# Kernel optimization log

Measured on AMD Instinct MI355X. Metric: run time of the kernel, lower is better.

The kernel has to match this reference:

```python
import jax, jax.numpy as jnp
import numpy as np

N = 16000      # nodes
E = 256000     # edges (avg degree 16)
C = 64         # channel multiplicity (64x0e node feats)
A = 10         # num elements (one-hot node_attrs)
R = 8          # num radial edge feats
OFFS = [0, 1, 4, 9]   # m-offsets for l=0,1,2 blocks (dims 1,3,5)
AVG_NEIGH = 16.0


def setup_inputs() -> dict:
    key = jax.random.key(0)
    ks = jax.random.split(key, 12)
    species = jax.random.randint(ks[0], (N,), 0, A)
    node_attrs = jax.nn.one_hot(species, A, dtype=jnp.float32)
    node_feats = jax.random.normal(ks[1], (N, C), jnp.float32)
    edge_attrs_real = jax.random.normal(ks[2], (E, 9), jnp.float32)
    edge_attrs_imag = jax.random.normal(ks[3], (E, 9), jnp.float32)
    edge_feats = jax.random.normal(ks[4], (E, R), jnp.float32)
    senders = jax.random.randint(ks[5], (E,), 0, N)
    receivers = jax.random.randint(ks[6], (E,), 0, N)
    # learned parameters
    W_up = jax.random.normal(ks[7], (C, C), jnp.float32)            # linear_up (64x0e -> 64x0e)
    W_tpw = jax.random.normal(ks[8], (A, R, 3, C), jnp.float32) * 0.1  # TensorProductWeightsBlock, weight_numel = 3*C
    W_lin = jax.random.normal(ks[9], (3, C, C), jnp.float32)        # per-l linear on irreps_mid -> irreps_out
    W_skip = jax.random.normal(ks[10], (C, A, C), jnp.float32)      # FullyConnectedTensorProduct skip
    return {"node_attrs": node_attrs, "node_feats": node_feats,
            "edge_attrs_real": edge_attrs_real, "edge_attrs_imag": edge_attrs_imag,
            "edge_feats": edge_feats, "senders": senders, "receivers": receivers,
            "W_up": W_up, "W_tpw": W_tpw, "W_lin": W_lin, "W_skip": W_skip}


def reference(node_attrs, node_feats, edge_attrs_real, edge_attrs_imag, edge_feats,
              senders, receivers, W_up, W_tpw, W_lin, W_skip):
    # skip connection: FullyConnectedTensorProduct(node_feats, node_attrs) (all scalars)
    sc = jnp.einsum('nu,na,uak->nk', node_feats, node_attrs, W_skip) / np.float32(np.sqrt(C * A))
    # linear_up (e3nn Linear with 1/sqrt(fan_in) normalization)
    h = (node_feats @ W_up) / np.float32(np.sqrt(C))
    # per-edge TP weights: einsum('be,ba,aek->bk'), reshaped to [E, 3 paths, C]
    tp_w = jnp.einsum('er,ea,arlu->elu', edge_feats, node_attrs[senders], W_tpw)
    x_s = h[senders]  # gather sender node feats [E, C]
    def conv(edge_attrs):
        # uvu tensor product 64x0e x (0e+1o+2e): CG(0,l,l)=1 -> weighted outer product per l
        parts = [x_s[:, :, None] * tp_w[:, l, :, None] * edge_attrs[:, None, OFFS[l]:OFFS[l + 1]]
                 for l in range(3)]
        mji = jnp.concatenate(parts, axis=-1)                      # [E, C, 9]
        m = jax.ops.segment_sum(mji, receivers, num_segments=N)   # scatter-sum -> [N, C, 9]
        outs = [jnp.einsum('num,uv->nvm', m[:, :, OFFS[l]:OFFS[l + 1]], W_lin[l]) / np.float32(np.sqrt(C))
                for l in range(3)]
        return jnp.concatenate(outs, axis=-1) / np.float32(AVG_NEIGH)  # [N, C, 9]
    message_real = conv(edge_attrs_real)
    message_imag = conv(edge_attrs_imag)
    # torch.view_as_complex + reshape_irreps -> complex [N, C, 9]; returned as (real, imag)
    return message_real, message_imag, sc
```

## Files before the change

kernel.cpp:

```cpp
#include <hip/hip_runtime.h>
#include <hip/hip_bf16.h>

#define NN 16000
#define EE 256000
#define CC 64
#define AA 10
#define RR 8
#define NC9 9216000
#define SC_OFF 18432000

#define WS_H        0
#define WS_BLK      4096000
#define WS_WLT      32768256
#define WS_SPECIES  32817408
#define WS_COUNTS   32881408
#define WS_CURSOR   32945408
#define WS_OFFSETS  33009408
#define WS_PERM     33073472
#define WS_DSTART   33137472
#define WS_DEGCUR   33137728

__device__ __forceinline__ float comp4(float4 v, int j) {
  return j == 0 ? v.x : j == 1 ? v.y : j == 2 ? v.z : v.w;
}

__global__ __launch_bounds__(256) void prep_kernel(
    const float* __restrict__ attrs, const int* __restrict__ recv,
    const float* __restrict__ W_lin, const float* __restrict__ nf,
    const float* __restrict__ W_up, const float* __restrict__ W_skip,
    int* __restrict__ species, int* __restrict__ counts,
    float* __restrict__ wlt, float* __restrict__ h, float* __restrict__ out) {
  __shared__ float sW[4096];
  for (int t = threadIdx.x; t < 4096; t += 256) sW[t] = W_up[t];
  __syncthreads();
  int i = blockIdx.x * 256 + threadIdx.x;
  if (i < NN) {
    const float* p = attrs + (size_t)i * AA;
    int sp = 0;
#pragma unroll
    for (int a = 1; a < AA; ++a)
      if (p[a] > 0.5f) sp = a;
    species[i] = sp;
  }
  if (i < 3 * 64 * 64) {
    int l = i >> 12, rem = i & 4095, v = rem >> 6, u = rem & 63;
    wlt[i] = W_lin[l * 4096 + u * 64 + v];
  }
  if (i < EE) atomicAdd(&counts[recv[i]], 1);
  int wid = __builtin_amdgcn_readfirstlane(threadIdx.x >> 6);
  int lane = threadIdx.x & 63;
  for (int n = blockIdx.x * 4 + wid; n < NN; n += 4000) {
    const float* ap = attrs + (size_t)n * AA;
    int a = 0;
#pragma unroll
    for (int j = 1; j < AA; ++j)
      if (ap[j] > 0.5f) a = j;
    const float* nfp = nf + (size_t)n * 64;
    const float* wsk = W_skip + (size_t)a * 64;
    float hacc = 0.f, sacc = 0.f;
#pragma unroll
    for (int u = 0; u < 64; ++u) {
      float x = nfp[u];
      hacc = fmaf(x, sW[u * 64 + lane], hacc);
      sacc = fmaf(x, wsk[u * 640 + lane], sacc);
    }
    h[(size_t)n * 64 + lane] = hacc * 0.125f;
    out[SC_OFF + (size_t)n * 64 + lane] = sacc * 0.03952847075210474f;
  }
}

__global__ __launch_bounds__(1024) void scan_kernel(
    const int* __restrict__ counts, int* __restrict__ offsets,
    int* __restrict__ dstart, int* __restrict__ degcur) {
  __shared__ int part[1024];
  __shared__ int hist[64];
  int tid = threadIdx.x;
  if (tid < 64) { hist[tid] = 0; degcur[tid] = 0; }
  const int CH = 16;
  int base = tid * CH;
  int loc[CH];
  int s = 0;
#pragma unroll
  for (int i = 0; i < CH; ++i) {
    int idx = base + i;
    int c = (idx < NN) ? counts[idx] : 0;
    loc[i] = c;
    s += c;
  }
  part[tid] = s;
  __syncthreads();
  for (int off = 1; off < 1024; off <<= 1) {
    int t = part[tid];
    int add = (tid >= off) ? part[tid - off] : 0;
    __syncthreads();
    part[tid] = t + add;
    __syncthreads();
  }
  int pre = (tid > 0) ? part[tid - 1] : 0;
#pragma unroll
  for (int i = 0; i < CH; ++i) {
    int idx = base + i;
    if (idx <= NN) offsets[idx] = pre;
    pre += loc[i];
    if (idx < NN) atomicAdd(&hist[min(loc[i], 63)], 1);
  }
  __syncthreads();
  if (tid == 0) {
    int run = 0;
    for (int d = 63; d >= 0; --d) { dstart[d] = run; run += hist[d]; }
  }
}

__global__ __launch_bounds__(256) void edge_kernel(
    const int* __restrict__ recv, const int* __restrict__ senders,
    const int* __restrict__ species, const int* __restrict__ offsets,
    int* __restrict__ cursor, const int* __restrict__ counts,
    const int* __restrict__ dstart, int* __restrict__ degcur,
    int* __restrict__ perm, const float* __restrict__ ef,
    const float* __restrict__ ear, const float* __restrict__ eai,
    float* __restrict__ blk) {
  int e = blockIdx.x * 256 + threadIdx.x;
  if (e < NN) {
    int d = min(counts[e], 63);
    int pos = atomicAdd(&degcur[d], 1);
    perm[dstart[d] + pos] = e;
  }
  if (e >= EE) return;
  int r = recv[e];
  int pos = atomicAdd(&cursor[r], 1);
  int slot = offsets[r] + pos;
  int s = senders[e];
  int a = species[s];
  const float* efp = ef + (size_t)e * 8;
  const float* erp = ear + (size_t)e * 9;
  const float* eip = eai + (size_t)e * 9;
  float4* dst = (float4*)(blk + (size_t)slot * 28);
  float4 q;
  q.x = __int_as_float(s | (a << 20)); q.y = efp[0]; q.z = efp[1]; q.w = efp[2];
  dst[0] = q;
  q.x = efp[3]; q.y = efp[4]; q.z = efp[5]; q.w = efp[6];
  dst[1] = q;
  q.x = efp[7]; q.y = erp[0]; q.z = erp[1]; q.w = erp[2];
  dst[2] = q;
  q.x = erp[3]; q.y = erp[4]; q.z = erp[5]; q.w = erp[6];
  dst[3] = q;
  q.x = erp[7]; q.y = erp[8]; q.z = eip[0]; q.w = eip[1];
  dst[4] = q;
  q.x = eip[2]; q.y = eip[3]; q.z = eip[4]; q.w = eip[5];
  dst[5] = q;
  q.x = eip[6]; q.y = eip[7]; q.z = eip[8]; q.w = 0.f;
  dst[6] = q;
}

#define RLF(V, L) __int_as_float(__builtin_amdgcn_readlane((V), (L)))

#define EDGE2(EFA, ERA, EIA, PKV, XS) do {                                 \
  int a_ = (PKV) >> 20;                                                    \
  const float4* wp_ = (const float4*)(lds + a_ * 1792 + lane * 28);        \
  float4 w_[6];                                                            \
  _Pragma("unroll") for (int g_ = 0; g_ < 6; ++g_) w_[g_] = wp_[gpi[g_]];  \
  float t0_ = 0.f, t1_ = 0.f, t2_ = 0.f;                                   \
  _Pragma("unroll") for (int r_ = 0; r_ < 8; ++r_) {                       \
    t0_ = fmaf((EFA)[r_], comp4(w_[(r_ * 3 + 0) >> 2], (r_ * 3 + 0) & 3), t0_); \
    t1_ = fmaf((EFA)[r_], comp4(w_[(r_ * 3 + 1) >> 2], (r_ * 3 + 1) & 3), t1_); \
    t2_ = fmaf((EFA)[r_], comp4(w_[(r_ * 3 + 2) >> 2], (r_ * 3 + 2) & 3), t2_); \
  }                                                                        \
  t0_ *= (XS); t1_ *= (XS); t2_ *= (XS);                                   \
  accR[0] = fmaf(t0_, (ERA)[0], accR[0]);                                  \
  accI[0] = fmaf(t0_, (EIA)[0], accI[0]);                                  \
  _Pragma("unroll") for (int m_ = 1; m_ < 4; ++m_) {                       \
    accR[m_] = fmaf(t1_, (ERA)[m_], accR[m_]);                             \
    accI[m_] = fmaf(t1_, (EIA)[m_], accI[m_]);                             \
  }                                                                        \
  _Pragma("unroll") for (int m_ = 4; m_ < 9; ++m_) {                       \
    accR[m_] = fmaf(t2_, (ERA)[m_], accR[m_]);                             \
    accI[m_] = fmaf(t2_, (EIA)[m_], accI[m_]);                             \
  }                                                                        \
} while (0)

#define MIXL(LV, M0, M1)                                                    \
  _Pragma("unroll") for (int q_ = 0; q_ < 16; ++q_) {                       \
    float4 w4_ = *(const float4*)&lds[(LV) * 4096 + lane * 64 +             \
                                      ((q_ + lane) & 15) * 4];              \
    _Pragma("unroll") for (int j_ = 0; j_ < 4; ++j_) {                      \
      float wu_ = comp4(w4_, j_);                                           \
      _Pragma("unroll") for (int m_ = (M0); m_ < (M1); ++m_) {              \
        outR[m_] = fmaf(RLF(__float_as_int(accR[m_]), q_ * 4 + j_), wu_, outR[m_]); \
        outI[m_] = fmaf(RLF(__float_as_int(accI[m_]), q_ * 4 + j_), wu_, outI[m_]); \
      }                                                                     \
    }                                                                       \
  }

__global__ __launch_bounds__(512, 4) void fused_kernel(
    const float* __restrict__ h, const int* __restrict__ offs,
    const float* __restrict__ blkd, const int* __restrict__ perm,
    const float* __restrict__ W_tpw, const float* __restrict__ wlt,
    float* __restrict__ out) {
  __shared__ float lds[17920];
  for (int t = threadIdx.x; t < AA * 6 * 64; t += 512) {
    int a = t / 384, rem = t - a * 384;
    int g = rem >> 6, u = rem & 63;
    int gp = (g + 5 * u) % 7;
    const float* src = W_tpw + a * 1536 + g * 256 + u;
    float4 w;
    w.x = src[0]; w.y = src[64]; w.z = src[128]; w.w = src[192];
    *(float4*)&lds[a * 1792 + u * 28 + gp * 4] = w;
  }
  __syncthreads();
  int wid = __builtin_amdgcn_readfirstlane(threadIdx.x >> 6);
  int lane = threadIdx.x & 63;
  int n = __builtin_amdgcn_readfirstlane(perm[blockIdx.x * 8 + wid]);
  int gpi[6];
#pragma unroll
  for (int g = 0; g < 6; ++g) gpi[g] = (g + 5 * lane) % 7;
  float accR[9], accI[9];
#pragma unroll
  for (int m = 0; m < 9; ++m) { accR[m] = 0.f; accI[m] = 0.f; }
  int beg = __builtin_amdgcn_readfirstlane(offs[n]);
  int end_ = __builtin_amdgcn_readfirstlane(offs[n + 1]);
  if (end_ > beg) {
    const int* bi = (const int*)blkd;
    int pk0 = bi[(size_t)beg * 28];
    int pk1 = (beg + 1 < end_) ? bi[(size_t)(beg + 1) * 28] : pk0;
    float xs0 = h[(size_t)(pk0 & 0xFFFFF) * 64 + lane];
    float xs1 = h[(size_t)(pk1 & 0xFFFFF) * 64 + lane];
    float efc[8], erc[9], eic[9];
    {
      const float* ep = blkd + (size_t)beg * 28;
#pragma unroll
      for (int i = 0; i < 8; ++i) efc[i] = ep[1 + i];
#pragma unroll
      for (int i = 0; i < 9; ++i) erc[i] = ep[9 + i];
#pragma unroll
      for (int i = 0; i < 9; ++i) eic[i] = ep[18 + i];
    }
    for (int idx = beg; idx < end_; ++idx) {
      int pk2 = pk0;
      float xs2 = 0.f;
      if (idx + 2 < end_) {
        pk2 = bi[(size_t)(idx + 2) * 28];
        xs2 = h[(size_t)(pk2 & 0xFFFFF) * 64 + lane];
      }
      float efn[8], ern[9], ein[9];
      if (idx + 1 < end_) {
        const float* ep = blkd + (size_t)(idx + 1) * 28;
#pragma unroll
        for (int i = 0; i < 8; ++i) efn[i] = ep[1 + i];
#pragma unroll
        for (int i = 0; i < 9; ++i) ern[i] = ep[9 + i];
#pragma unroll
        for (int i = 0; i < 9; ++i) ein[i] = ep[18 + i];
      } else {
#pragma unroll
        for (int i = 0; i < 8; ++i) efn[i] = 0.f;
#pragma unroll
        for (int i = 0; i < 9; ++i) { ern[i] = 0.f; ein[i] = 0.f; }
      }
      EDGE2(efc, erc, eic, pk0, xs0);
      pk0 = pk1; xs0 = xs1;
      pk1 = pk2; xs1 = xs2;
#pragma unroll
      for (int i = 0; i < 8; ++i) efc[i] = efn[i];
#pragma unroll
      for (int i = 0; i < 9; ++i) { erc[i] = ern[i]; eic[i] = ein[i]; }
    }
  }
  __builtin_amdgcn_sched_barrier(0);
  __syncthreads();
  for (int t = threadIdx.x; t < 3072; t += 512) {
    int l = t >> 10, rem = t & 1023, v = rem >> 4, q = rem & 15;
    int slot = (q + v) & 15;
    float4 w = *(const float4*)(wlt + l * 4096 + v * 64 + q * 4);
    *(float4*)&lds[l * 4096 + v * 64 + slot * 4] = w;
  }
  __syncthreads();
  float outR[9], outI[9];
#pragma unroll
  for (int m = 0; m < 9; ++m) { outR[m] = 0.f; outI[m] = 0.f; }
  MIXL(0, 0, 1)
  MIXL(1, 1, 4)
  MIXL(2, 4, 9)
  const float SCL = 0.0078125f;
  float* stg = lds + 12288 + wid * 576;
#pragma unroll
  for (int m = 0; m < 9; ++m) stg[lane * 9 + m] = outR[m] * SCL;
  __builtin_amdgcn_s_waitcnt(0);
#pragma unroll
  for (int k = 0; k < 9; ++k)
    out[(size_t)n * 576 + k * 64 + lane] = stg[k * 64 + lane];
#pragma unroll
  for (int m = 0; m < 9; ++m) stg[lane * 9 + m] = outI[m] * SCL;
  __builtin_amdgcn_s_waitcnt(0);
#pragma unroll
  for (int k = 0; k < 9; ++k)
    out[NC9 + (size_t)n * 576 + k * 64 + lane] = stg[k * 64 + lane];
}

extern "C" void kernel_launch(void* const* d_in, const int* in_sizes, int n_in,
                              void* d_out, int out_size, void* d_ws, size_t ws_size,
                              hipStream_t stream) {
  const float* node_attrs = (const float*)d_in[0];
  const float* node_feats = (const float*)d_in[1];
  const float* ear        = (const float*)d_in[2];
  const float* eai        = (const float*)d_in[3];
  const float* ef         = (const float*)d_in[4];
  const int*   senders    = (const int*)d_in[5];
  const int*   receivers  = (const int*)d_in[6];
  const float* W_up       = (const float*)d_in[7];
  const float* W_tpw      = (const float*)d_in[8];
  const float* W_lin      = (const float*)d_in[9];
  const float* W_skip     = (const float*)d_in[10];
  float* out = (float*)d_out;

  char* ws = (char*)d_ws;
  float* h        = (float*)(ws + WS_H);
  float* blk      = (float*)(ws + WS_BLK);
  float* wlt      = (float*)(ws + WS_WLT);
  int*   species  = (int*)(ws + WS_SPECIES);
  int*   counts   = (int*)(ws + WS_COUNTS);
  int*   cursor   = (int*)(ws + WS_CURSOR);
  int*   offsets  = (int*)(ws + WS_OFFSETS);
  int*   perm     = (int*)(ws + WS_PERM);
  int*   dstart   = (int*)(ws + WS_DSTART);
  int*   degcur   = (int*)(ws + WS_DEGCUR);

  hipMemsetAsync(ws + WS_COUNTS, 0, 128000, stream);

  prep_kernel<<<1000, 256, 0, stream>>>(node_attrs, receivers, W_lin,
                                        node_feats, W_up, W_skip,
                                        species, counts, wlt, h, out);
  scan_kernel<<<1, 1024, 0, stream>>>(counts, offsets, dstart, degcur);
  edge_kernel<<<1000, 256, 0, stream>>>(receivers, senders, species, offsets,
                                        cursor, counts, dstart, degcur, perm,
                                        ef, ear, eai, blk);
  fused_kernel<<<2000, 512, 0, stream>>>(h, offsets, blk, perm, W_tpw, wlt,
                                         out);
}
```

Measured before the change: 351.6 us.

## Replace packed per-edge block with edge index and gather edge data in fused kernel

The edge kernel no longer copies edge features and edge attributes into a 28-float sorted block. It writes only an (edge id, sender|species) pair per slot, and the fused kernel reads ef/ear/eai directly by edge id, broadcasting them with readfirstlane. This cuts the write and re-read of about 28 MB of staging data, but turns the fused kernel's edge reads into scattered, non-sequential loads and drops the software prefetch of edge data. The change also splits the node linear/skip work into its own one-wave-per-node kernel, drops the LDS swizzle on the TP weights, and adds a sync in the scan kernel.

```diff
diff --git a/kernel.cpp b/kernel.cpp
--- a/kernel.cpp
+++ b/kernel.cpp
@@ -10,29 +10,27 @@
 #define SC_OFF 18432000
 
 #define WS_H        0
-#define WS_BLK      4096000
-#define WS_WLT      32768256
-#define WS_SPECIES  32817408
-#define WS_COUNTS   32881408
-#define WS_CURSOR   32945408
-#define WS_OFFSETS  33009408
-#define WS_PERM     33073472
-#define WS_DSTART   33137472
-#define WS_DEGCUR   33137728
+#define WS_EP2      4096000
+#define WS_WLT      6144000
+#define WS_SPECIES  6193152
+#define WS_COUNTS   6257152
+#define WS_CURSOR   6321152
+#define WS_OFFSETS  6385152
+#define WS_PERM     6449216
+#define WS_DSTART   6513216
+#define WS_DEGCUR   6513472
 
 __device__ __forceinline__ float comp4(float4 v, int j) {
   return j == 0 ? v.x : j == 1 ? v.y : j == 2 ? v.z : v.w;
 }
+__device__ __forceinline__ float rflf(float v) {
+  return __int_as_float(__builtin_amdgcn_readfirstlane(__float_as_int(v)));
+}
 
 __global__ __launch_bounds__(256) void prep_kernel(
     const float* __restrict__ attrs, const int* __restrict__ recv,
-    const float* __restrict__ W_lin, const float* __restrict__ nf,
-    const float* __restrict__ W_up, const float* __restrict__ W_skip,
-    int* __restrict__ species, int* __restrict__ counts,
-    float* __restrict__ wlt, float* __restrict__ h, float* __restrict__ out) {
-  __shared__ float sW[4096];
-  for (int t = threadIdx.x; t < 4096; t += 256) sW[t] = W_up[t];
-  __syncthreads();
+    const float* __restrict__ W_lin, int* __restrict__ species,
+    int* __restrict__ counts, float* __restrict__ wlt) {
   int i = blockIdx.x * 256 + threadIdx.x;
   if (i < NN) {
     const float* p = attrs + (size_t)i * AA;
@@ -47,26 +45,35 @@
     wlt[i] = W_lin[l * 4096 + u * 64 + v];
   }
   if (i < EE) atomicAdd(&counts[recv[i]], 1);
+}
+
+__global__ __launch_bounds__(256) void node_kernel(
+    const float* __restrict__ nf, const float* __restrict__ attrs,
+    const float* __restrict__ W_up, const float* __restrict__ W_skip,
+    float* __restrict__ h, float* __restrict__ out) {
+  __shared__ float sW[4096];
+  for (int t = threadIdx.x; t < 4096; t += 256) sW[t] = W_up[t];
+  __syncthreads();
   int wid = __builtin_amdgcn_readfirstlane(threadIdx.x >> 6);
   int lane = threadIdx.x & 63;
-  for (int n = blockIdx.x * 4 + wid; n < NN; n += 4000) {
-    const float* ap = attrs + (size_t)n * AA;
-    int a = 0;
-#pragma unroll
-    for (int j = 1; j < AA; ++j)
-      if (ap[j] > 0.5f) a = j;
-    const float* nfp = nf + (size_t)n * 64;
-    const float* wsk = W_skip + (size_t)a * 64;
-    float hacc = 0.f, sacc = 0.f;
-#pragma unroll
-    for (int u = 0; u < 64; ++u) {
-      float x = nfp[u];
-      hacc = fmaf(x, sW[u * 64 + lane], hacc);
-      sacc = fmaf(x, wsk[u * 640 + lane], sacc);
-    }
-    h[(size_t)n * 64 + lane] = hacc * 0.125f;
-    out[SC_OFF + (size_t)n * 64 + lane] = sacc * 0.03952847075210474f;
-  }
+  int n = blockIdx.x * 4 + wid;
+  if (n >= NN) return;
+  const float* ap = attrs + (size_t)n * AA;
+  int a = 0;
+#pragma unroll
+  for (int j = 1; j < AA; ++j)
+    if (ap[j] > 0.5f) a = j;
+  const float* nfp = nf + (size_t)n * 64;
+  const float* wsk = W_skip + (size_t)a * 64;
+  float hacc = 0.f, sacc = 0.f;
+#pragma unroll
+  for (int u = 0; u < 64; ++u) {
+    float x = nfp[u];
+    hacc = fmaf(x, sW[u * 64 + lane], hacc);
+    sacc = fmaf(x, wsk[u * 640 + lane], sacc);
+  }
+  h[(size_t)n * 64 + lane] = hacc * 0.125f;
+  out[SC_OFF + (size_t)n * 64 + lane] = sacc * 0.03952847075210474f;
 }
 
 __global__ __launch_bounds__(1024) void scan_kernel(
@@ -76,6 +83,7 @@
   __shared__ int hist[64];
   int tid = threadIdx.x;
   if (tid < 64) { hist[tid] = 0; degcur[tid] = 0; }
+  __syncthreads();
   const int CH = 16;
   int base = tid * CH;
   int loc[CH];
@@ -116,9 +124,7 @@
     const int* __restrict__ species, const int* __restrict__ offsets,
     int* __restrict__ cursor, const int* __restrict__ counts,
     const int* __restrict__ dstart, int* __restrict__ degcur,
-    int* __restrict__ perm, const float* __restrict__ ef,
-    const float* __restrict__ ear, const float* __restrict__ eai,
-    float* __restrict__ blk) {
+    int* __restrict__ perm, int2* __restrict__ ep2) {
   int e = blockIdx.x * 256 + threadIdx.x;
   if (e < NN) {
     int d = min(counts[e], 63);
@@ -131,52 +137,42 @@
   int slot = offsets[r] + pos;
   int s = senders[e];
   int a = species[s];
-  const float* efp = ef + (size_t)e * 8;
-  const float* erp = ear + (size_t)e * 9;
-  const float* eip = eai + (size_t)e * 9;
-  float4* dst = (float4*)(blk + (size_t)slot * 28);
-  float4 q;
-  q.x = __int_as_float(s | (a << 20)); q.y = efp[0]; q.z = efp[1]; q.w = efp[2];
-  dst[0] = q;
-  q.x = efp[3]; q.y = efp[4]; q.z = efp[5]; q.w = efp[6];
-  dst[1] = q;
-  q.x = efp[7]; q.y = erp[0]; q.z = erp[1]; q.w = erp[2];
-  dst[2] = q;
-  q.x = erp[3]; q.y = erp[4]; q.z = erp[5]; q.w = erp[6];
-  dst[3] = q;
-  q.x = erp[7]; q.y = erp[8]; q.z = eip[0]; q.w = eip[1];
-  dst[4] = q;
-  q.x = eip[2]; q.y = eip[3]; q.z = eip[4]; q.w = eip[5];
-  dst[5] = q;
-  q.x = eip[6]; q.y = eip[7]; q.z = eip[8]; q.w = 0.f;
-  dst[6] = q;
-}
-
-#define RLF(V, L) __int_as_float(__builtin_amdgcn_readlane((V), (L)))
-
-#define EDGE2(EFA, ERA, EIA, PKV, XS) do {                                 \
-  int a_ = (PKV) >> 20;                                                    \
+  ep2[slot] = make_int2(e, s | (a << 20));
+}
+
+#define EDGE3(RC, XS) do {                                                 \
+  int e_ = (RC).x;                                                         \
+  int a_ = (RC).y >> 20;                                                   \
+  const float* efp_ = ef + (size_t)e_ * 8;          \
+  const float* erp_ = ear + (size_t)e_ * 9;                                \
+  const float* eip_ = eai + (size_t)e_ * 9;                                \
+  float efs_[8], ers_[9], eis_[9];                                         \
+  _Pragma("unroll") for (int i_ = 0; i_ < 8; ++i_) efs_[i_] = rflf(efp_[i_]); \
+  _Pragma("unroll") for (int i_ = 0; i_ < 9; ++i_) ers_[i_] = rflf(erp_[i_]); \
+  _Pragma("unroll") for (int i_ = 0; i_ < 9; ++i_) eis_[i_] = rflf(eip_[i_]); \
   const float4* wp_ = (const float4*)(lds + a_ * 1792 + lane * 28);        \
   float4 w_[6];                                                            \
-  _Pragma("unroll") for (int g_ = 0; g_ < 6; ++g_) w_[g_] = wp_[gpi[g_]];  \
+  _Pragma("unroll") for (int g_ = 0; g_ < 6; ++g_) w_[g_] = wp_[g_];       \
   float t0_ = 0.f, t1_ = 0.f, t2_ = 0.f;                                   \
   _Pragma("unroll") for (int r_ = 0; r_ < 8; ++r_) {                       \
-    t0_ = fmaf((EFA)[r_], comp4(w_[(r_ * 3 + 0) >> 2], (r_ * 3 + 0) & 3), t0_); \
-    t1_ = fmaf((EFA)[r_], comp4(w_[(r_ * 3 + 1) >> 2], (r_ * 3 + 1) & 3), t1_); \
-    t2_ = fmaf((EFA)[r_], comp4(w_[(r_ * 3 + 2) >> 2], (r_ * 3 + 2) & 3), t2_); \
+    t0_ = fmaf(efs_[r_], comp4(w_[(r_ * 3 + 0) >> 2], (r_ * 3 + 0) & 3), t0_); \
+    t1_ = fmaf(efs_[r_], comp4(w_[(r_ * 3 + 1) >> 2], (r_ * 3 + 1) & 3), t1_); \
+    t2_ = fmaf(efs_[r_], comp4(w_[(r_ * 3 + 2) >> 2], (r_ * 3 + 2) & 3), t2_); \
   }                                                                        \
   t0_ *= (XS); t1_ *= (XS); t2_ *= (XS);                                   \
-  accR[0] = fmaf(t0_, (ERA)[0], accR[0]);                                  \
-  accI[0] = fmaf(t0_, (EIA)[0], accI[0]);                                  \
+  accR[0] = fmaf(t0_, ers_[0], accR[0]);                                   \
+  accI[0] = fmaf(t0_, eis_[0], accI[0]);                                   \
   _Pragma("unroll") for (int m_ = 1; m_ < 4; ++m_) {                       \
-    accR[m_] = fmaf(t1_, (ERA)[m_], accR[m_]);                             \
-    accI[m_] = fmaf(t1_, (EIA)[m_], accI[m_]);                             \
+    accR[m_] = fmaf(t1_, ers_[m_], accR[m_]);                              \
+    accI[m_] = fmaf(t1_, eis_[m_], accI[m_]);                              \
   }                                                                        \
   _Pragma("unroll") for (int m_ = 4; m_ < 9; ++m_) {                       \
-    accR[m_] = fmaf(t2_, (ERA)[m_], accR[m_]);                             \
-    accI[m_] = fmaf(t2_, (EIA)[m_], accI[m_]);                             \
+    accR[m_] = fmaf(t2_, ers_[m_], accR[m_]);                              \
+    accI[m_] = fmaf(t2_, eis_[m_], accI[m_]);                              \
   }                                                                        \
 } while (0)
+
+#define RLF(V, L) __int_as_float(__builtin_amdgcn_readlane((V), (L)))
 
 #define MIXL(LV, M0, M1)                                                    \
   _Pragma("unroll") for (int q_ = 0; q_ < 16; ++q_) {                       \
@@ -193,76 +189,43 @@
 
 __global__ __launch_bounds__(512, 4) void fused_kernel(
     const float* __restrict__ h, const int* __restrict__ offs,
-    const float* __restrict__ blkd, const int* __restrict__ perm,
-    const float* __restrict__ W_tpw, const float* __restrict__ wlt,
-    float* __restrict__ out) {
+    const int2* __restrict__ ep2, const int* __restrict__ perm,
+    const float* __restrict__ ef, const float* __restrict__ ear,
+    const float* __restrict__ eai, const float* __restrict__ W_tpw,
+    const float* __restrict__ wlt, float* __restrict__ out) {
   __shared__ float lds[17920];
   for (int t = threadIdx.x; t < AA * 6 * 64; t += 512) {
     int a = t / 384, rem = t - a * 384;
     int g = rem >> 6, u = rem & 63;
-    int gp = (g + 5 * u) % 7;
     const float* src = W_tpw + a * 1536 + g * 256 + u;
     float4 w;
     w.x = src[0]; w.y = src[64]; w.z = src[128]; w.w = src[192];
-    *(float4*)&lds[a * 1792 + u * 28 + gp * 4] = w;
+    *(float4*)&lds[a * 1792 + u * 28 + g * 4] = w;
   }
   __syncthreads();
   int wid = __builtin_amdgcn_readfirstlane(threadIdx.x >> 6);
   int lane = threadIdx.x & 63;
   int n = __builtin_amdgcn_readfirstlane(perm[blockIdx.x * 8 + wid]);
-  int gpi[6];
-#pragma unroll
-  for (int g = 0; g < 6; ++g) gpi[g] = (g + 5 * lane) % 7;
   float accR[9], accI[9];
 #pragma unroll
   for (int m = 0; m < 9; ++m) { accR[m] = 0.f; accI[m] = 0.f; }
   int beg = __builtin_amdgcn_readfirstlane(offs[n]);
   int end_ = __builtin_amdgcn_readfirstlane(offs[n + 1]);
   if (end_ > beg) {
-    const int* bi = (const int*)blkd;
-    int pk0 = bi[(size_t)beg * 28];
-    int pk1 = (beg + 1 < end_) ? bi[(size_t)(beg + 1) * 28] : pk0;
-    float xs0 = h[(size_t)(pk0 & 0xFFFFF) * 64 + lane];
-    float xs1 = h[(size_t)(pk1 & 0xFFFFF) * 64 + lane];
-    float efc[8], erc[9], eic[9];
-    {
-      const float* ep = blkd + (size_t)beg * 28;
-#pragma unroll
-      for (int i = 0; i < 8; ++i) efc[i] = ep[1 + i];
-#pragma unroll
-      for (int i = 0; i < 9; ++i) erc[i] = ep[9 + i];
-#pragma unroll
-      for (int i = 0; i < 9; ++i) eic[i] = ep[18 + i];
-    }
+    int2 r0 = ep2[beg];
+    int2 r1 = (beg + 1 < end_) ? ep2[beg + 1] : r0;
+    float xs0 = h[(size_t)(r0.y & 0xFFFFF) * 64 + lane];
+    float xs1 = h[(size_t)(r1.y & 0xFFFFF) * 64 + lane];
     for (int idx = beg; idx < end_; ++idx) {
-      int pk2 = pk0;
+      int2 r2 = r0;
       float xs2 = 0.f;
       if (idx + 2 < end_) {
-        pk2 = bi[(size_t)(idx + 2) * 28];
-        xs2 = h[(size_t)(pk2 & 0xFFFFF) * 64 + lane];
+        r2 = ep2[idx + 2];
+        xs2 = h[(size_t)(r2.y & 0xFFFFF) * 64 + lane];
       }
-      float efn[8], ern[9], ein[9];
-      if (idx + 1 < end_) {
-        const float* ep = blkd + (size_t)(idx + 1) * 28;
-#pragma unroll
-        for (int i = 0; i < 8; ++i) efn[i] = ep[1 + i];
-#pragma unroll
-        for (int i = 0; i < 9; ++i) ern[i] = ep[9 + i];
-#pragma unroll
-        for (int i = 0; i < 9; ++i) ein[i] = ep[18 + i];
-      } else {
-#pragma unroll
-        for (int i = 0; i < 8; ++i) efn[i] = 0.f;
-#pragma unroll
-        for (int i = 0; i < 9; ++i) { ern[i] = 0.f; ein[i] = 0.f; }
-      }
-      EDGE2(efc, erc, eic, pk0, xs0);
-      pk0 = pk1; xs0 = xs1;
-      pk1 = pk2; xs1 = xs2;
-#pragma unroll
-      for (int i = 0; i < 8; ++i) efc[i] = efn[i];
-#pragma unroll
-      for (int i = 0; i < 9; ++i) { erc[i] = ern[i]; eic[i] = ein[i]; }
+      EDGE3(r0, xs0);
+      r0 = r1; xs0 = xs1;
+      r1 = r2; xs1 = xs2;
     }
   }
   __builtin_amdgcn_sched_barrier(0);
@@ -314,7 +277,7 @@
 
   char* ws = (char*)d_ws;
   float* h        = (float*)(ws + WS_H);
-  float* blk      = (float*)(ws + WS_BLK);
+  int2*  ep2      = (int2*)(ws + WS_EP2);
   float* wlt      = (float*)(ws + WS_WLT);
   int*   species  = (int*)(ws + WS_SPECIES);
   int*   counts   = (int*)(ws + WS_COUNTS);
@@ -327,12 +290,13 @@
   hipMemsetAsync(ws + WS_COUNTS, 0, 128000, stream);
 
   prep_kernel<<<1000, 256, 0, stream>>>(node_attrs, receivers, W_lin,
-                                        node_feats, W_up, W_skip,
-                                        species, counts, wlt, h, out);
+                                        species, counts, wlt);
+  node_kernel<<<4000, 256, 0, stream>>>(node_feats, node_attrs, W_up, W_skip,
+                                        h, out);
   scan_kernel<<<1, 1024, 0, stream>>>(counts, offsets, dstart, degcur);
   edge_kernel<<<1000, 256, 0, stream>>>(receivers, senders, species, offsets,
                                         cursor, counts, dstart, degcur, perm,
-                                        ef, ear, eai, blk);
-  fused_kernel<<<2000, 512, 0, stream>>>(h, offsets, blk, perm, W_tpw, wlt,
-                                         out);
-}
+                                        ep2);
+  fused_kernel<<<2000, 512, 0, stream>>>(h, offsets, ep2, perm, ef, ear, eai,
+                                         W_tpw, wlt, out);
+}
```

After: 339.2 us. -3.5%, faster.
